# Optimization experiments

Measured on AMD Instinct MI355X. Metric: run time of the kernel, lower is better.

Reference implementation:

```python
import jax, jax.numpy as jnp
import numpy as np

N = 8192
D = 128
NUM_INSTANCES = 8  # samples per class (balanced PK batch)
ALPHA = 50.0
BASE = 1.0


def setup_inputs() -> dict:
    key = jax.random.key(0)
    k1, = jax.random.split(key, 1)
    x = jax.random.normal(k1, (N, D), dtype=jnp.float32)
    # L2-normalize so pairwise dists ~ sqrt(2) and exp(alpha*(1-d)) stays finite in fp32
    inputs = x / jnp.linalg.norm(x, axis=1, keepdims=True)
    targets = (jnp.arange(N) // NUM_INSTANCES).astype(jnp.int64)
    return {"inputs": inputs, "targets": targets}


def _euclidean_dist(x):
    sq = jnp.sum(x * x, axis=1)  # [n]
    d2 = sq[:, None] + sq[None, :] - 2.0 * (x @ x.T)  # [n, n]
    return jnp.sqrt(jnp.clip(d2, 1e-12, None))


def reference(inputs, targets):
    n = inputs.shape[0]
    dist = _euclidean_dist(inputs)                      # [n, n]
    same = targets[:, None] == targets[None, :]         # [n, n] bool
    eye = jnp.eye(n, dtype=bool)
    pos_mask = same & ~eye                              # positives, excluding self
    neg_mask = ~same                                    # negatives

    e = jnp.exp(ALPHA * (BASE - dist))                  # [n, n]
    pos_logit = jnp.sum(jnp.where(pos_mask, e, 0.0), axis=1)        # [n]
    neg_logit = jnp.sum(jnp.where(neg_mask, e, 0.0), axis=1) * 0.5  # [n]
    loss = jnp.mean(-jnp.log(pos_logit / (pos_logit + neg_logit)))

    pos_d = jnp.sum(jnp.where(pos_mask, dist, 0.0)) / jnp.sum(pos_mask)
    neg_d = jnp.sum(jnp.where(neg_mask, dist, 0.0)) / jnp.sum(neg_mask)
    prec = jnp.float32(1.0)  # err is always 0 in the original code
    return (loss, prec, pos_d, neg_d)
```

## Files before the change

kernel.cpp:

```cpp
#include <hip/hip_runtime.h>

#define NN 8192
#define DD 128
#define C2 72.13475204444817f
#define LN2 0.6931471805599453f
#define NTILE 64
#define NTRI 2080
#define NBLK 512

typedef __attribute__((ext_vector_type(8))) __bf16 bf16x8;
typedef __attribute__((ext_vector_type(4))) float f32x4;

#if __has_builtin(__builtin_amdgcn_exp2f)
#define EXP2F(x) __builtin_amdgcn_exp2f(x)
#else
#define EXP2F(x) exp2f(x)
#endif
#if __has_builtin(__builtin_amdgcn_sqrtf)
#define SQRTF(x) __builtin_amdgcn_sqrtf(x)
#else
#define SQRTF(x) sqrtf(x)
#endif
#if __has_builtin(__builtin_amdgcn_logf)
#define LOG2F(x) __builtin_amdgcn_logf(x)
#else
#define LOG2F(x) log2f(x)
#endif

__device__ __forceinline__ unsigned short f2bf(float f) {
  unsigned u = __float_as_uint(f);
  u += 0x7FFFu + ((u >> 16) & 1u);
  return (unsigned short)(u >> 16);
}

__device__ __forceinline__ void gload_lds16(const void* g, void* l) {
  __builtin_amdgcn_global_load_lds(
      (const __attribute__((address_space(1))) void*)g,
      (__attribute__((address_space(3))) void*)l, 16, 0, 0);
}

__device__ __forceinline__ float dpp_row_sum16(float v) {
  v += __int_as_float(__builtin_amdgcn_update_dpp(
      0, __float_as_int(v), 0x121, 0xf, 0xf, true));
  v += __int_as_float(__builtin_amdgcn_update_dpp(
      0, __float_as_int(v), 0x122, 0xf, 0xf, true));
  v += __int_as_float(__builtin_amdgcn_update_dpp(
      0, __float_as_int(v), 0x124, 0xf, 0xf, true));
  v += __int_as_float(__builtin_amdgcn_update_dpp(
      0, __float_as_int(v), 0x128, 0xf, 0xf, true));
  return v;
}
__device__ __forceinline__ float wave_sum64(float v) {
  v = dpp_row_sum16(v);
  v += __shfl_xor(v, 16, 64);
  v += __shfl_xor(v, 32, 64);
  return v;
}

__global__ __launch_bounds__(512) void prep_pos_kernel(
    const float* __restrict__ x, unsigned short* __restrict__ xbf,
    float* __restrict__ pos_e, float* __restrict__ pos_d,
    float* __restrict__ accs, unsigned* __restrict__ cnt) {
  int w = threadIdx.x >> 6;
  int lane = threadIdx.x & 63;
  int i = blockIdx.x * 8 + w;

  __shared__ float xs[8][128];
  __shared__ float sqs[8];

  const float* xr = x + (size_t)i * DD;
  float a = xr[lane], b = xr[lane + 64];
  xs[w][lane] = a;
  xs[w][lane + 64] = b;

  float s = wave_sum64(__fmaf_rn(a, a, b * b));
  if (lane == 0) sqs[w] = s;
  unsigned short* o = xbf + (size_t)i * DD;
  int t1 = lane >> 3, e1 = lane & 7;
  o[((t1 ^ w) << 3) + e1] = f2bf(a);
  o[64 + ((t1 ^ w) << 3) + e1] = f2bf(b);
  if (blockIdx.x == 0) {
    if (threadIdx.x == 0) {
      accs[0] = 0.f;
      accs[1] = 0.f;
      accs[2] = 0.f;
    }
    if (threadIdx.x == 1) cnt[0] = 0u;
  }

  __syncthreads();
  float sqi = sqs[w];
  float pe = 0.f, pd = 0.f;
  for (int j = 0; j < 8; ++j) {
    if (j == w) continue;
    float dot =
        wave_sum64(__fmaf_rn(a, xs[j][lane], b * xs[j][lane + 64]));
    float d2 = fmaxf(__fmaf_rn(-2.f, dot, sqi + sqs[j]), 1e-12f);
    float dist = SQRTF(d2);
    pe += EXP2F(__fmaf_rn(dist, -C2, C2));
    pd += dist;
  }
  if (lane == 0) {
    pos_e[i] = pe;
    pos_d[i] = pd;
  }
}

__global__ __launch_bounds__(512, 4) void tile_kernel(
    const unsigned short* __restrict__ xbf, float* __restrict__ part,
    float* __restrict__ dpart) {
  int lane = threadIdx.x & 63;
  int wave = threadIdx.x >> 6;
  int q = lane >> 4, c = lane & 15;
  int rh = wave >> 2, cq = wave & 3;

  int k0 = (65 * blockIdx.x) >> 4, k1 = (65 * (blockIdx.x + 1)) >> 4;
  int tr = (int)((129.0f - SQRTF(16641.0f - 8.0f * (float)k0)) * 0.5f);
  while (tr > 0 && tr * (129 - tr) / 2 > k0) --tr;
  while ((tr + 1) * (128 - tr) / 2 <= k0) ++tr;
  int tc = tr + (k0 - tr * (129 - tr) / 2);

  __shared__ char panelB[65536];
  __shared__ float rowsumW[2][4][128];
  __shared__ float colsumW[2][2][128];
  __shared__ float partd[8];

  int swz8 = (c & 7);
  int goffB = wave * 4096 + lane * 16;

  bf16x8 ar[4][4];
  int atr = tr;
  float dacc = 0.f;

  {
    int I0p = tr * 128 + rh * 64;
#pragma unroll
    for (int rb = 0; rb < 4; ++rb) {
      const unsigned short* rp = xbf + (size_t)(I0p + rb * 16 + c) * DD;
#pragma unroll
      for (int ks = 0; ks < 4; ++ks)
        ar[rb][ks] = *(const bf16x8*)(rp + (((ks * 4 + q) ^ swz8) << 3));
    }
  }

  {
    const char* gB = (const char*)xbf + (size_t)tc * 32768;
    char* lB = panelB + wave * 4096;
#pragma unroll
    for (int t = 0; t < 4; ++t) gload_lds16(gB + t * 1024 + goffB, lB + t * 1024);
  }

  __syncthreads();

  for (int k = k0; k < k1; ++k) {
    int cur = (k - k0) & 1;
    int I0 = tr * 128 + rh * 64;
    int J0 = tc * 128 + cq * 32;
    bool diag = (tr == tc);

    if (atr != tr) {
      atr = tr;
#pragma unroll
      for (int rb = 0; rb < 4; ++rb) {
        const unsigned short* rp = xbf + (size_t)(I0 + rb * 16 + c) * DD;
#pragma unroll
        for (int ks = 0; ks < 4; ++ks)
          ar[rb][ks] = *(const bf16x8*)(rp + (((ks * 4 + q) ^ swz8) << 3));
      }
    }

    if (k + 1 < k1) {
      int tcn = (tc + 1 < 64) ? tc + 1 : tr + 1;
      const char* gB = (const char*)xbf + (size_t)tcn * 32768;
      char* lB = panelB + (cur ^ 1) * 32768 + wave * 4096;
#pragma unroll
      for (int t = 0; t < 4; ++t)
        gload_lds16(gB + t * 1024 + goffB, lB + t * 1024);
    }

    f32x4 acc[4][2];
#pragma unroll
    for (int rb = 0; rb < 4; ++rb)
#pragma unroll
      for (int cb = 0; cb < 2; ++cb)
        acc[rb][cb] = (f32x4){0.f, 0.f, 0.f, 0.f};

    {
      const char* pb = panelB + cur * 32768 + cq * 8192 + c * 256;
#pragma unroll
      for (int ks = 0; ks < 4; ++ks) {
        int koff = (ks * 64 + q * 16) ^ (swz8 << 4);
        bf16x8 br[2];
#pragma unroll
        for (int cb = 0; cb < 2; ++cb)
          br[cb] = *(const bf16x8*)(pb + cb * 4096 + koff);
#pragma unroll
        for (int rb = 0; rb < 4; ++rb)
#pragma unroll
          for (int cb = 0; cb < 2; ++cb)
            acc[rb][cb] = __builtin_amdgcn_mfma_f32_16x16x32_bf16(
                ar[rb][ks], br[cb], acc[rb][cb], 0, 0, 0);
      }
    }

    float tote[16];
#pragma unroll
    for (int kk = 0; kk < 16; ++kk) tote[kk] = 0.f;
    float pcol[2] = {0.f, 0.f};
    float totd = 0.f;

    if (!diag) {
#pragma unroll
      for (int rb = 0; rb < 4; ++rb) {
#pragma unroll
        for (int cb = 0; cb < 2; ++cb) {
#pragma unroll
          for (int r = 0; r < 4; ++r) {
            float d2 = __fmaf_rn(-2.f, acc[rb][cb][r], 2.0f);
            float dist = SQRTF(d2);
            float ex = EXP2F(__fmaf_rn(dist, -C2, C2));
            tote[rb * 4 + r] += ex;
            pcol[cb] += ex;
            totd += dist;
          }
        }
      }
      dacc += 2.f * totd;
    } else {
#pragma unroll
      for (int rb = 0; rb < 4; ++rb) {
#pragma unroll
        for (int cb = 0; cb < 2; ++cb) {
          bool diagSub = (rh * 4 + rb) == (cq * 2 + cb);
#pragma unroll
          for (int r = 0; r < 4; ++r) {
            float d2 = __fmaf_rn(-2.f, acc[rb][cb][r], 2.0f);
            float dist = SQRTF(d2);
            float ex = EXP2F(__fmaf_rn(dist, -C2, C2));
            if (diagSub && (q * 4 + r) == c) {
              ex = 0.f;
              dist = 0.f;
            }
            tote[rb * 4 + r] += ex;
            totd += dist;
          }
        }
      }
      dacc += totd;
    }

#pragma unroll
    for (int kk = 0; kk < 16; ++kk) tote[kk] = dpp_row_sum16(tote[kk]);
    if (c == 0) {
#pragma unroll
      for (int rb = 0; rb < 4; ++rb)
#pragma unroll
        for (int r = 0; r < 4; ++r)
          rowsumW[cur][cq][rh * 64 + rb * 16 + q * 4 + r] = tote[rb * 4 + r];
    }
    if (!diag) {
#pragma unroll
      for (int cb = 0; cb < 2; ++cb) {
        float cs = pcol[cb];
        cs += __shfl_xor(cs, 16, 64);
        cs += __shfl_xor(cs, 32, 64);
        if (q == 0) colsumW[cur][rh][cq * 32 + cb * 16 + c] = cs;
      }
    }

    __syncthreads();

    size_t rslot = ((size_t)tr * NTILE + tc) * 128;
    size_t cslot = ((size_t)tc * NTILE + tr) * 128;
    int t = threadIdx.x;
    if (t < 128) {
      part[rslot + t] = rowsumW[cur][0][t] + rowsumW[cur][1][t] +
                        rowsumW[cur][2][t] + rowsumW[cur][3][t];
    } else if (t < 256 && !diag) {
      int t2 = t - 128;
      part[cslot + t2] = colsumW[cur][0][t2] + colsumW[cur][1][t2];
    }
    if (tc + 1 < 64) {
      ++tc;
    } else {
      ++tr;
      tc = tr;
    }
  }

  dacc = wave_sum64(dacc);
  if (lane == 0) partd[wave] = dacc;
  __syncthreads();
  if (threadIdx.x == 0) {
    float sacc = 0.f;
#pragma unroll
    for (int w2 = 0; w2 < 8; ++w2) sacc += partd[w2];
    dpart[blockIdx.x] = sacc;
  }
}

__global__ __launch_bounds__(128) void fin_kernel(
    const float* __restrict__ part, const float* __restrict__ dpart,
    const float* __restrict__ pos_e, const float* __restrict__ pos_d,
    float* accs, unsigned* cnt, float* __restrict__ out) {
  int a = blockIdx.x, c = threadIdx.x;
  const float* pa = part + (size_t)a * NTILE * 128 + c;
  float tot = 0.f;
#pragma unroll
  for (int t = 0; t < 64; ++t) tot += pa[(size_t)t * 128];
  int i = a * 128 + c;
  float p = pos_e[i];
  float denom = __fmaf_rn(0.5f, tot - p, p);
  float lsum = LOG2F(denom) - LOG2F(p);
  float pdsum = pos_d[i];
  float ds = (c < 8) ? dpart[a * 8 + c] : 0.f;

  __shared__ float s1[128], s2[128], s3[128];
  s1[c] = lsum;
  s2[c] = pdsum;
  s3[c] = ds;
  __syncthreads();
  for (int w = 64; w; w >>= 1) {
    if (c < w) {
      s1[c] += s1[c + w];
      s2[c] += s2[c + w];
      s3[c] += s3[c + w];
    }
    __syncthreads();
  }
  if (c == 0) {
    atomicAdd(&accs[0], s1[0]);
    atomicAdd(&accs[1], s2[0]);
    atomicAdd(&accs[2], s3[0]);
    __threadfence();
    unsigned old = atomicAdd(cnt, 1u);
    if (old == 63u) {
      float L = atomicAdd(&accs[0], 0.f);
      float PD = atomicAdd(&accs[1], 0.f);
      float DS = atomicAdd(&accs[2], 0.f);
      out[0] = L * LN2 / (float)NN;
      out[1] = 1.0f;
      out[2] = PD / (float)(NN * 7);
      out[3] = (DS - PD) / ((float)NN * 8184.f);
    }
  }
}

extern "C" void kernel_launch(void* const* d_in, const int* in_sizes, int n_in,
                              void* d_out, int out_size, void* d_ws,
                              size_t ws_size, hipStream_t stream) {
  const float* x = (const float*)d_in[0];
  float* out = (float*)d_out;
  char* ws = (char*)d_ws;

  unsigned short* xbf = (unsigned short*)ws;
  float* pos_e = (float*)(ws + (size_t)NN * DD * 2);
  float* pos_d = pos_e + NN;
  float* part = pos_d + NN;
  float* dpart = part + (size_t)NTILE * NTILE * 128;
  float* accs = dpart + NBLK;
  unsigned* cnt = (unsigned*)(accs + 3);

  prep_pos_kernel<<<NN / 8, 512, 0, stream>>>(x, xbf, pos_e, pos_d, accs, cnt);
  tile_kernel<<<NBLK, 512, 0, stream>>>(xbf, part, dpart);
  fin_kernel<<<64, 128, 0, stream>>>(part, dpart, pos_e, pos_d, accs, cnt,
                                     out);
}
```

Baseline: 112.0 us.

## Use 4-wave blocks with 64x64 per-wave tiles and double the block count

The tile kernel now runs 256-thread blocks (4 waves), each wave computing a 64x64 sub-tile with 16 MFMA accumulators instead of 64x32, and the grid grows to 1024 blocks, each covering half as many 128x128 triangle tiles. Each wave loads twice as much of the B panel into LDS, and the final kernel reduces 16 distance partials per row block. The aim is more register-level reuse of the A fragments, more independent blocks for load balance, and less reduction overhead in shared memory. In exchange, the doubled accumulator set raises register pressure and may lower occupancy, and LDS use per block stays at 64 KB.

```diff
diff --git a/kernel.cpp b/kernel.cpp
--- a/kernel.cpp
+++ b/kernel.cpp
@@ -6,7 +6,7 @@
 #define LN2 0.6931471805599453f
 #define NTILE 64
 #define NTRI 2080
-#define NBLK 512
+#define NBLK 1024
 
 typedef __attribute__((ext_vector_type(8))) __bf16 bf16x8;
 typedef __attribute__((ext_vector_type(4))) float f32x4;
@@ -106,34 +106,34 @@
   }
 }
 
-__global__ __launch_bounds__(512, 4) void tile_kernel(
+__global__ __launch_bounds__(256, 2) void tile_kernel(
     const unsigned short* __restrict__ xbf, float* __restrict__ part,
     float* __restrict__ dpart) {
   int lane = threadIdx.x & 63;
   int wave = threadIdx.x >> 6;
   int q = lane >> 4, c = lane & 15;
-  int rh = wave >> 2, cq = wave & 3;
-
-  int k0 = (65 * blockIdx.x) >> 4, k1 = (65 * (blockIdx.x + 1)) >> 4;
+  int rw = wave >> 1, cw = wave & 1;
+
+  int k0 = (65 * blockIdx.x) >> 5, k1 = (65 * (blockIdx.x + 1)) >> 5;
   int tr = (int)((129.0f - SQRTF(16641.0f - 8.0f * (float)k0)) * 0.5f);
   while (tr > 0 && tr * (129 - tr) / 2 > k0) --tr;
   while ((tr + 1) * (128 - tr) / 2 <= k0) ++tr;
   int tc = tr + (k0 - tr * (129 - tr) / 2);
 
   __shared__ char panelB[65536];
-  __shared__ float rowsumW[2][4][128];
+  __shared__ float rowsumW[2][2][128];
   __shared__ float colsumW[2][2][128];
-  __shared__ float partd[8];
+  __shared__ float partd[4];
 
   int swz8 = (c & 7);
-  int goffB = wave * 4096 + lane * 16;
+  int goffB = wave * 8192 + lane * 16;
 
   bf16x8 ar[4][4];
   int atr = tr;
   float dacc = 0.f;
 
   {
-    int I0p = tr * 128 + rh * 64;
+    int I0p = tr * 128 + rw * 64;
 #pragma unroll
     for (int rb = 0; rb < 4; ++rb) {
       const unsigned short* rp = xbf + (size_t)(I0p + rb * 16 + c) * DD;
@@ -145,17 +145,17 @@
 
   {
     const char* gB = (const char*)xbf + (size_t)tc * 32768;
-    char* lB = panelB + wave * 4096;
-#pragma unroll
-    for (int t = 0; t < 4; ++t) gload_lds16(gB + t * 1024 + goffB, lB + t * 1024);
+    char* lB = panelB + wave * 8192;
+#pragma unroll
+    for (int t = 0; t < 8; ++t) gload_lds16(gB + t * 1024 + goffB, lB + t * 1024);
   }
 
   __syncthreads();
 
   for (int k = k0; k < k1; ++k) {
     int cur = (k - k0) & 1;
-    int I0 = tr * 128 + rh * 64;
-    int J0 = tc * 128 + cq * 32;
+    int I0 = tr * 128 + rw * 64;
+    int J0 = tc * 128 + cw * 64;
     bool diag = (tr == tc);
 
     if (atr != tr) {
@@ -172,32 +172,32 @@
     if (k + 1 < k1) {
       int tcn = (tc + 1 < 64) ? tc + 1 : tr + 1;
       const char* gB = (const char*)xbf + (size_t)tcn * 32768;
-      char* lB = panelB + (cur ^ 1) * 32768 + wave * 4096;
-#pragma unroll
-      for (int t = 0; t < 4; ++t)
+      char* lB = panelB + (cur ^ 1) * 32768 + wave * 8192;
+#pragma unroll
+      for (int t = 0; t < 8; ++t)
         gload_lds16(gB + t * 1024 + goffB, lB + t * 1024);
     }
 
-    f32x4 acc[4][2];
+    f32x4 acc[4][4];
 #pragma unroll
     for (int rb = 0; rb < 4; ++rb)
 #pragma unroll
-      for (int cb = 0; cb < 2; ++cb)
+      for (int cb = 0; cb < 4; ++cb)
         acc[rb][cb] = (f32x4){0.f, 0.f, 0.f, 0.f};
 
     {
-      const char* pb = panelB + cur * 32768 + cq * 8192 + c * 256;
+      const char* pb = panelB + cur * 32768 + cw * 16384 + c * 256;
 #pragma unroll
       for (int ks = 0; ks < 4; ++ks) {
         int koff = (ks * 64 + q * 16) ^ (swz8 << 4);
-        bf16x8 br[2];
-#pragma unroll
-        for (int cb = 0; cb < 2; ++cb)
+        bf16x8 br[4];
+#pragma unroll
+        for (int cb = 0; cb < 4; ++cb)
           br[cb] = *(const bf16x8*)(pb + cb * 4096 + koff);
 #pragma unroll
         for (int rb = 0; rb < 4; ++rb)
 #pragma unroll
-          for (int cb = 0; cb < 2; ++cb)
+          for (int cb = 0; cb < 4; ++cb)
             acc[rb][cb] = __builtin_amdgcn_mfma_f32_16x16x32_bf16(
                 ar[rb][ks], br[cb], acc[rb][cb], 0, 0, 0);
       }
@@ -206,14 +206,14 @@
     float tote[16];
 #pragma unroll
     for (int kk = 0; kk < 16; ++kk) tote[kk] = 0.f;
-    float pcol[2] = {0.f, 0.f};
+    float pcol[4] = {0.f, 0.f, 0.f, 0.f};
     float totd = 0.f;
 
     if (!diag) {
 #pragma unroll
       for (int rb = 0; rb < 4; ++rb) {
 #pragma unroll
-        for (int cb = 0; cb < 2; ++cb) {
+        for (int cb = 0; cb < 4; ++cb) {
 #pragma unroll
           for (int r = 0; r < 4; ++r) {
             float d2 = __fmaf_rn(-2.f, acc[rb][cb][r], 2.0f);
@@ -230,8 +230,8 @@
 #pragma unroll
       for (int rb = 0; rb < 4; ++rb) {
 #pragma unroll
-        for (int cb = 0; cb < 2; ++cb) {
-          bool diagSub = (rh * 4 + rb) == (cq * 2 + cb);
+        for (int cb = 0; cb < 4; ++cb) {
+          bool diagSub = (I0 + rb * 16) == (J0 + cb * 16);
 #pragma unroll
           for (int r = 0; r < 4; ++r) {
             float d2 = __fmaf_rn(-2.f, acc[rb][cb][r], 2.0f);
@@ -256,15 +256,15 @@
       for (int rb = 0; rb < 4; ++rb)
 #pragma unroll
         for (int r = 0; r < 4; ++r)
-          rowsumW[cur][cq][rh * 64 + rb * 16 + q * 4 + r] = tote[rb * 4 + r];
+          rowsumW[cur][cw][rw * 64 + rb * 16 + q * 4 + r] = tote[rb * 4 + r];
     }
     if (!diag) {
 #pragma unroll
-      for (int cb = 0; cb < 2; ++cb) {
+      for (int cb = 0; cb < 4; ++cb) {
         float cs = pcol[cb];
         cs += __shfl_xor(cs, 16, 64);
         cs += __shfl_xor(cs, 32, 64);
-        if (q == 0) colsumW[cur][rh][cq * 32 + cb * 16 + c] = cs;
+        if (q == 0) colsumW[cur][rw][cw * 64 + cb * 16 + c] = cs;
       }
     }
 
@@ -274,9 +274,8 @@
     size_t cslot = ((size_t)tc * NTILE + tr) * 128;
     int t = threadIdx.x;
     if (t < 128) {
-      part[rslot + t] = rowsumW[cur][0][t] + rowsumW[cur][1][t] +
-                        rowsumW[cur][2][t] + rowsumW[cur][3][t];
-    } else if (t < 256 && !diag) {
+      part[rslot + t] = rowsumW[cur][0][t] + rowsumW[cur][1][t];
+    } else if (!diag) {
       int t2 = t - 128;
       part[cslot + t2] = colsumW[cur][0][t2] + colsumW[cur][1][t2];
     }
@@ -291,12 +290,8 @@
   dacc = wave_sum64(dacc);
   if (lane == 0) partd[wave] = dacc;
   __syncthreads();
-  if (threadIdx.x == 0) {
-    float sacc = 0.f;
-#pragma unroll
-    for (int w2 = 0; w2 < 8; ++w2) sacc += partd[w2];
-    dpart[blockIdx.x] = sacc;
-  }
+  if (threadIdx.x == 0)
+    dpart[blockIdx.x] = partd[0] + partd[1] + partd[2] + partd[3];
 }
 
 __global__ __launch_bounds__(128) void fin_kernel(
@@ -313,7 +308,7 @@
   float denom = __fmaf_rn(0.5f, tot - p, p);
   float lsum = LOG2F(denom) - LOG2F(p);
   float pdsum = pos_d[i];
-  float ds = (c < 8) ? dpart[a * 8 + c] : 0.f;
+  float ds = (c < 16) ? dpart[a * 16 + c] : 0.f;
 
   __shared__ float s1[128], s2[128], s3[128];
   s1[c] = lsum;
@@ -362,7 +357,7 @@
   unsigned* cnt = (unsigned*)(accs + 3);
 
   prep_pos_kernel<<<NN / 8, 512, 0, stream>>>(x, xbf, pos_e, pos_d, accs, cnt);
-  tile_kernel<<<NBLK, 512, 0, stream>>>(xbf, part, dpart);
+  tile_kernel<<<NBLK, 256, 0, stream>>>(xbf, part, dpart);
   fin_kernel<<<64, 128, 0, stream>>>(part, dpart, pos_e, pos_d, accs, cnt,
                                      out);
 }
```

Result: faster. 97.09 us (-13.3%).
